# Kernel optimization log

Hardware: AMD Instinct MI355X
Metric: run time of the kernel (lower is better)

Reference implementation:

```python
import jax, jax.numpy as jnp
import numpy as np


def setup_inputs() -> dict:
    key = jax.random.key(0)
    k1, k2 = jax.random.split(key)
    input = jax.random.normal(k1, (4, 2048, 2048), dtype=jnp.float32)
    target = jax.random.normal(k2, (4, 2048, 2048), dtype=jnp.float32) * 2.0 + 0.5
    return {"input": input, "target": target}


def _hist_match(source, template):
    """JAX histogram matching, equivalent to the numpy unique/cumsum/interp
    version for inputs with distinct values (true for continuous random data).

    For each source element x, its empirical quantile is
        q(x) = count(source <= x) / N  == s_quantiles[bin_idx] in the numpy code,
    computed via sort + searchsorted(side='right').
    The template CDF is the sorted template paired with quantiles (j+1)/M,
    matching cumsum(t_counts)/M at each (unique) value.
    """
    src = source.ravel()
    tmpl_sorted = jnp.sort(template.ravel())
    N = src.shape[0]
    M = tmpl_sorted.shape[0]
    s_sorted = jnp.sort(src)
    # rank of each element among all source elements (count <= x)
    ranks = jnp.searchsorted(s_sorted, src, side='right')
    s_q = ranks.astype(jnp.float32) / jnp.float32(N)
    t_q = jnp.arange(1, M + 1, dtype=jnp.float32) / jnp.float32(M)
    matched = jnp.interp(s_q, t_q, tmpl_sorted)
    return matched.reshape(source.shape)


def reference(input, target):
    # hist_match_torch.forward: matched histogram (non-differentiable in original)
    matched = jax.lax.stop_gradient(_hist_match(input, target))
    # HistogramLoss: (matched - input)^2 summed / numel
    loss = jnp.mean((matched - input) ** 2)
    # original forward returns `input`; the meaningful computed quantities are
    # the matched tensor and the loss, so we return both.
    return matched, loss
```

## Files before the change

### kernel.cpp

```cpp
#include <hip/hip_runtime.h>
#include <cstdint>


#define NBINS    8192u
#define HGX      640u
#define MGX      2048u
#define KIN      2048u
#define KTG      4096u

__device__ __forceinline__ void bin_and_frac(float x, unsigned& b, float& frac) {
    float d = __builtin_fmaf(x, 256.0f, 4096.0f);
    d = fminf(fmaxf(d, 0.0f), 8191.999f);
    unsigned bb = (unsigned)d;
    b = bb;
    frac = d - (float)bb;
}

__global__ void hist_kernel(const float* __restrict__ in, const float* __restrict__ tg,
                            unsigned* __restrict__ H, unsigned n8) {
    __shared__ unsigned h[NBINS];
    for (unsigned i = threadIdx.x; i < NBINS; i += 256) h[i] = 0;
    __syncthreads();
    const float* x = blockIdx.y ? tg : in;
    unsigned* Hh = H + blockIdx.y * NBINS;
    unsigned stride = gridDim.x * 256;
    for (unsigned i = blockIdx.x * 256 + threadIdx.x; i < n8; i += stride) {
        float4 a0 = ((const float4*)x)[2 * i];
        float4 a1 = ((const float4*)x)[2 * i + 1];
        float xs[8] = {a0.x, a0.y, a0.z, a0.w, a1.x, a1.y, a1.z, a1.w};
        #pragma unroll
        for (int k = 0; k < 8; k++) {
            unsigned b; float f;
            bin_and_frac(xs[k], b, f);
            atomicAdd(&h[b], 1u);
        }
    }
    __syncthreads();
    for (unsigned i = threadIdx.x; i < NBINS; i += 256) {
        unsigned v = h[i];
        if (v) atomicAdd(&Hh[i], v);
    }
}

__global__ void scan_kernel(const unsigned* __restrict__ H, unsigned* __restrict__ C) {
    __shared__ unsigned s[1024];
    const unsigned* h = H + blockIdx.x * NBINS;
    unsigned* c = C + blockIdx.x * (NBINS + 1);
    unsigned base = threadIdx.x * 8;
    unsigned v[8]; unsigned own = 0;
    #pragma unroll
    for (int k = 0; k < 8; k++) { v[k] = h[base + k]; own += v[k]; }
    s[threadIdx.x] = own; __syncthreads();
    for (unsigned off = 1; off < 1024; off <<= 1) {
        unsigned t = (threadIdx.x >= off) ? s[threadIdx.x - off] : 0u;
        __syncthreads();
        s[threadIdx.x] += t;
        __syncthreads();
    }
    unsigned ex = s[threadIdx.x] - own;
    #pragma unroll
    for (int k = 0; k < 8; k++) { unsigned t = v[k]; c[base + k] = ex; ex += t; }
    if (threadIdx.x == 1023) c[NBINS] = s[1023];
}

__global__ void buildAB_kernel(const unsigned* __restrict__ Cin, const unsigned* __restrict__ Ctg,
                               float2* __restrict__ AB, int* __restrict__ hdr, unsigned n) {
    unsigned b = blockIdx.x * blockDim.x + threadIdx.x;
    if (b >= NBINS) return;
    unsigned r0 = Cin[b], r1 = Cin[b + 1];
    if (r1 <= KIN) atomicMax(&hdr[0], (int)b);
    if (r0 >= n - KIN) atomicMin(&hdr[1], (int)b);
    unsigned t0 = Ctg[b], t1 = Ctg[b + 1];
    if (t1 <= KTG) atomicMax(&hdr[2], (int)b);
    if (t0 >= n - KTG) atomicMin(&hdr[3], (int)b);
    if (r1 == r0) { AB[b] = make_float2(0.f, 0.f); return; }
    const float w = 32.0f / (float)NBINS;
    float v[2];
    unsigned rr[2] = {r0, r1};
    #pragma unroll
    for (int k = 0; k < 2; k++) {
        unsigned r = rr[k]; if (r > n - 1) r = n - 1;
        unsigned lo = 0, hi = NBINS;
        while (hi - lo > 1) { unsigned mid = (lo + hi) >> 1; if (Ctg[mid] <= r) lo = mid; else hi = mid; }
        unsigned c0 = Ctg[lo], c1 = Ctg[lo + 1];
        v[k] = -16.0f + (float)lo * w + w * ((float)(r - c0 + 1) / (float)(c1 - c0));
    }
    AB[b] = make_float2(v[0], v[1] - v[0]);
}

__global__ void exact_target_kernel(const float* __restrict__ tg_lo, const float* __restrict__ tg_hi,
                                    const unsigned* __restrict__ ctrs,
                                    float* __restrict__ Tlo, float* __restrict__ Thi) {
    __shared__ __align__(16) float v[KTG];
    int side = blockIdx.y;
    const float* src = side ? tg_hi : tg_lo;
    unsigned m = ctrs[side ? 3 : 2];
    if (m > KTG) m = KTG;
    float sgn = side ? -1.f : 1.f;
    for (unsigned k = threadIdx.x; k < m; k += 1024) v[k] = sgn * src[k];
    __syncthreads();
    unsigned j = blockIdx.x * 1024 + threadIdx.x;
    if (j >= m) return;
    float y = v[j];
    unsigned lt = 0, le = 0;
    unsigned m4 = m & ~3u;
    for (unsigned k = 0; k < m4; k += 4) {
        float4 z = *(const float4*)&v[k];
        lt += (z.x < y) + (z.y < y) + (z.z < y) + (z.w < y);
        le += (z.x <= y) + (z.y <= y) + (z.z <= y) + (z.w <= y);
    }
    for (unsigned k = m4; k < m; k++) { lt += (v[k] < y); le += (v[k] <= y); }
    float yo = sgn * y;
    if (side) {
        for (unsigned idx = KTG - le; idx < KTG - lt; idx++) Thi[idx] = yo;
    } else {
        for (unsigned r = lt; r < le; r++) Tlo[r] = yo;
    }
}

__global__ void matchcollect_kernel(const float* __restrict__ input, const float* __restrict__ target,
                                    const float2* __restrict__ AB, const int* __restrict__ hdr,
                                    float* __restrict__ vlo, unsigned* __restrict__ ilo,
                                    float* __restrict__ vhi, unsigned* __restrict__ ihi,
                                    float* __restrict__ tg_lo, float* __restrict__ tg_hi,
                                    unsigned* __restrict__ ctrs,
                                    float* __restrict__ out, float* __restrict__ bpart,
                                    unsigned n) {
    unsigned n8 = n >> 3;
    unsigned stride = gridDim.x * 256;
    unsigned i0 = blockIdx.x * 256 + threadIdx.x;

    if (blockIdx.y == 1) {
        int blo = hdr[2], bhi = hdr[3];
        for (unsigned i = i0; i < n8; i += stride) {
            float4 a0 = ((const float4*)target)[2 * i];
            float4 a1 = ((const float4*)target)[2 * i + 1];
            float xs[8] = {a0.x, a0.y, a0.z, a0.w, a1.x, a1.y, a1.z, a1.w};
            unsigned b[8];
            bool lo8[8], hi8[8];
            bool any = false;
            #pragma unroll
            for (int k = 0; k < 8; k++) {
                float f;
                bin_and_frac(xs[k], b[k], f);
                lo8[k] = ((int)b[k] <= blo);
                hi8[k] = ((int)b[k] >= bhi);
                any = any || lo8[k] || hi8[k];
            }
            if (any) {
                #pragma unroll
                for (int k = 0; k < 8; k++) {
                    if (lo8[k]) { unsigned p = atomicAdd(&ctrs[2], 1u); tg_lo[p] = xs[k]; }
                    else if (hi8[k]) { unsigned p = atomicAdd(&ctrs[3], 1u); tg_hi[p] = xs[k]; }
                }
            }
        }
        return;
    }

    int blo = hdr[0], bhi = hdr[1];
    float acc = 0.f;
    for (unsigned i = i0; i < n8; i += stride) {
        float4 a0 = ((const float4*)input)[2 * i];
        float4 a1 = ((const float4*)input)[2 * i + 1];
        float xs[8] = {a0.x, a0.y, a0.z, a0.w, a1.x, a1.y, a1.z, a1.w};
        unsigned b[8]; float fr[8];
        #pragma unroll
        for (int k = 0; k < 8; k++) bin_and_frac(xs[k], b[k], fr[k]);
        float2 ab[8];
        #pragma unroll
        for (int k = 0; k < 8; k++) ab[k] = AB[b[k]];
        bool tl[8]; bool any = false;
        #pragma unroll
        for (int k = 0; k < 8; k++) {
            tl[k] = ((int)b[k] <= blo) || ((int)b[k] >= bhi);
            any = any || tl[k];
        }
        float m[8];
        #pragma unroll
        for (int k = 0; k < 8; k++) {
            m[k] = __builtin_fmaf(ab[k].y, fr[k], ab[k].x);
            float d = tl[k] ? 0.f : (m[k] - xs[k]);
            acc = __builtin_fmaf(d, d, acc);
        }
        ((float4*)out)[2 * i]     = make_float4(m[0], m[1], m[2], m[3]);
        ((float4*)out)[2 * i + 1] = make_float4(m[4], m[5], m[6], m[7]);
        if (any) {
            #pragma unroll
            for (int k = 0; k < 8; k++) {
                if (!tl[k]) continue;
                if ((int)b[k] <= blo) { unsigned p = atomicAdd(&ctrs[0], 1u); vlo[p] = xs[k]; ilo[p] = 8 * i + k; }
                else                  { unsigned p = atomicAdd(&ctrs[1], 1u); vhi[p] = xs[k]; ihi[p] = 8 * i + k; }
            }
        }
    }
    #pragma unroll
    for (int off = 32; off > 0; off >>= 1) acc += __shfl_down(acc, off, 64);
    __shared__ float wsum[4];
    int wv = threadIdx.x >> 6;
    if ((threadIdx.x & 63) == 0) wsum[wv] = acc;
    __syncthreads();
    if (threadIdx.x == 0)
        bpart[blockIdx.x] = wsum[0] + wsum[1] + wsum[2] + wsum[3];
}

__global__ void loss_reduce_kernel(const float* __restrict__ bpart, float* __restrict__ loss,
                                   unsigned nb, unsigned n) {
    float s = 0.f;
    for (unsigned i = threadIdx.x; i < nb; i += 1024) s += bpart[i];
    #pragma unroll
    for (int off = 32; off > 0; off >>= 1) s += __shfl_down(s, off, 64);
    __shared__ float ws[16];
    int w = threadIdx.x >> 6;
    if ((threadIdx.x & 63) == 0) ws[w] = s;
    __syncthreads();
    if (threadIdx.x == 0) {
        float t = 0.f;
        #pragma unroll
        for (int k = 0; k < 16; k++) t += ws[k];
        *loss = t * (1.0f / (float)n);
    }
}

__global__ void exact_input_kernel(const float* __restrict__ in_lo_v, const unsigned* __restrict__ in_lo_i,
                                   const float* __restrict__ in_hi_v, const unsigned* __restrict__ in_hi_i,
                                   const unsigned* __restrict__ ctrs,
                                   const float* __restrict__ Tlo, const float* __restrict__ Thi,
                                   float* __restrict__ out, float* __restrict__ loss, unsigned n) {
    __shared__ __align__(16) float v[KIN];
    int side = blockIdx.y;
    const float* sv = side ? in_hi_v : in_lo_v;
    const unsigned* si = side ? in_hi_i : in_lo_i;
    unsigned m = ctrs[side ? 1 : 0];
    if (m > KIN) m = KIN;
    float sgn = side ? -1.f : 1.f;
    for (unsigned k = threadIdx.x; k < m; k += 1024) v[k] = sgn * sv[k];
    __syncthreads();
    unsigned j = blockIdx.x * 1024 + threadIdx.x;
    float d2 = 0.f;
    if (j < m) {
        float y = v[j];
        unsigned lt = 0, le = 0;
        unsigned m4 = m & ~3u;
        for (unsigned k = 0; k < m4; k += 4) {
            float4 z = *(const float4*)&v[k];
            lt += (z.x < y) + (z.y < y) + (z.z < y) + (z.w < y);
            le += (z.x <= y) + (z.y <= y) + (z.z <= y) + (z.w <= y);
        }
        for (unsigned k = m4; k < m; k++) { lt += (v[k] < y); le += (v[k] <= y); }
        float mv = side ? Thi[KTG - 1 - lt] : Tlo[le - 1];
        float x = sgn * y;
        out[si[j]] = mv;
        float d = mv - x;
        d2 = d * d;
    }
    #pragma unroll
    for (int off = 32; off > 0; off >>= 1) d2 += __shfl_down(d2, off, 64);
    if ((threadIdx.x & 63) == 0 && d2 != 0.f)
        atomicAdd(loss, d2 * (1.0f / (float)n));
}

extern "C" void kernel_launch(void* const* d_in, const int* in_sizes, int n_in,
                              void* d_out, int out_size, void* d_ws, size_t ws_size,
                              hipStream_t stream) {
    const float* input  = (const float*)d_in[0];
    const float* target = (const float*)d_in[1];
    unsigned n = (unsigned)in_sizes[0];
    float* out  = (float*)d_out;
    float* loss = out + n;

    char* wsb = (char*)d_ws;
    unsigned* H    = (unsigned*)(wsb);
    unsigned* Cin  = (unsigned*)(wsb + 64 * 1024);
    unsigned* Ctg  = Cin + (NBINS + 1);
    float2*   AB   = (float2*)  (wsb + 160 * 1024);
    int*      hdr  = (int*)     (wsb + 224 * 1024);
    unsigned* ctrs = (unsigned*)(wsb + 224 * 1024 + 64);
    float*    bpart= (float*)   (wsb + 224 * 1024 + 128);
    char*     tails= wsb + 240 * 1024;
    float*    in_lo_v = (float*)   (tails);
    unsigned* in_lo_i = (unsigned*)(tails + KIN * 4);
    float*    in_hi_v = (float*)   (tails + KIN * 8);
    unsigned* in_hi_i = (unsigned*)(tails + KIN * 12);
    float*    tg_lo   = (float*)   (tails + KIN * 16);
    float*    tg_hi   = (float*)   (tails + KIN * 16 + KTG * 4);
    float*    Tlo     = (float*)   (tails + KIN * 16 + KTG * 8);
    float*    Thi     = (float*)   (tails + KIN * 16 + KTG * 12);

    (void)hipMemsetAsync(H, 0, 2 * NBINS * 4, stream);
    (void)hipMemsetAsync(ctrs, 0, 16, stream);
    (void)hipMemsetAsync(&hdr[0], 0, 4, stream);
    (void)hipMemsetAsync(&hdr[1], 0x7F, 4, stream);
    (void)hipMemsetAsync(&hdr[2], 0, 4, stream);
    (void)hipMemsetAsync(&hdr[3], 0x7F, 4, stream);
    (void)hipMemsetAsync(loss, 0, 4, stream);

    unsigned n8 = n >> 3;

    hist_kernel<<<dim3(HGX, 2), 256, 0, stream>>>(input, target, H, n8);
    scan_kernel<<<2, 1024, 0, stream>>>(H, Cin);
    buildAB_kernel<<<NBINS / 256, 256, 0, stream>>>(Cin, Ctg, AB, hdr, n);

    matchcollect_kernel<<<dim3(MGX, 2), 256, 0, stream>>>(input, target, AB, hdr,
                                                          in_lo_v, in_lo_i, in_hi_v, in_hi_i,
                                                          tg_lo, tg_hi, ctrs, out, bpart, n);
    loss_reduce_kernel<<<1, 1024, 0, stream>>>(bpart, loss, MGX, n);
    exact_target_kernel<<<dim3((KTG + 1023) / 1024, 2), 1024, 0, stream>>>(tg_lo, tg_hi, ctrs, Tlo, Thi);
    exact_input_kernel<<<dim3((KIN + 1023) / 1024, 2), 1024, 0, stream>>>(in_lo_v, in_lo_i, in_hi_v, in_hi_i,
                                                                          ctrs, Tlo, Thi, out, loss, n);
}
```

Measured before the change: 538.2 us.

## Stage AB table in LDS, widen per-thread work, merge header memsets

The match kernel now copies the 8192-entry AB lookup table into shared memory once per block, so the per-element gathers hit LDS instead of global memory. Both the histogram and match kernels move to 512-thread blocks, each thread handling 16 elements, with smaller grids and launch bounds. The min-reductions in buildAB become max on 8192-b, which lets all header and counter fields be cleared with a single zero memset, and each wave writes its own loss partial without a block-level shared-memory reduction. The cost is a 64KB shared-memory fill per block and lower occupancy from the larger LDS footprint.

```diff
diff --git a/kernel.cpp b/kernel.cpp
--- a/kernel.cpp
+++ b/kernel.cpp
@@ -3,8 +3,8 @@
 
 
 #define NBINS    8192u
-#define HGX      640u
-#define MGX      2048u
+#define HGX      512u
+#define MGX      512u
 #define KIN      2048u
 #define KTG      4096u
 
@@ -16,27 +16,29 @@
     frac = d - (float)bb;
 }
 
-__global__ void hist_kernel(const float* __restrict__ in, const float* __restrict__ tg,
-                            unsigned* __restrict__ H, unsigned n8) {
+__global__ __launch_bounds__(512, 8) void hist_kernel(const float* __restrict__ in,
+                                                      const float* __restrict__ tg,
+                                                      unsigned* __restrict__ H, unsigned n16) {
     __shared__ unsigned h[NBINS];
-    for (unsigned i = threadIdx.x; i < NBINS; i += 256) h[i] = 0;
+    for (unsigned i = threadIdx.x; i < NBINS; i += 512) h[i] = 0;
     __syncthreads();
     const float* x = blockIdx.y ? tg : in;
     unsigned* Hh = H + blockIdx.y * NBINS;
-    unsigned stride = gridDim.x * 256;
-    for (unsigned i = blockIdx.x * 256 + threadIdx.x; i < n8; i += stride) {
-        float4 a0 = ((const float4*)x)[2 * i];
-        float4 a1 = ((const float4*)x)[2 * i + 1];
-        float xs[8] = {a0.x, a0.y, a0.z, a0.w, a1.x, a1.y, a1.z, a1.w};
-        #pragma unroll
-        for (int k = 0; k < 8; k++) {
+    unsigned stride = gridDim.x * 512;
+    for (unsigned i = blockIdx.x * 512 + threadIdx.x; i < n16; i += stride) {
+        const float4* p = (const float4*)x + 4u * i;
+        float4 a0 = p[0], a1 = p[1], a2 = p[2], a3 = p[3];
+        float xs[16] = {a0.x, a0.y, a0.z, a0.w, a1.x, a1.y, a1.z, a1.w,
+                        a2.x, a2.y, a2.z, a2.w, a3.x, a3.y, a3.z, a3.w};
+        #pragma unroll
+        for (int k = 0; k < 16; k++) {
             unsigned b; float f;
             bin_and_frac(xs[k], b, f);
             atomicAdd(&h[b], 1u);
         }
     }
     __syncthreads();
-    for (unsigned i = threadIdx.x; i < NBINS; i += 256) {
+    for (unsigned i = threadIdx.x; i < NBINS; i += 512) {
         unsigned v = h[i];
         if (v) atomicAdd(&Hh[i], v);
     }
@@ -69,10 +71,10 @@
     if (b >= NBINS) return;
     unsigned r0 = Cin[b], r1 = Cin[b + 1];
     if (r1 <= KIN) atomicMax(&hdr[0], (int)b);
-    if (r0 >= n - KIN) atomicMin(&hdr[1], (int)b);
+    if (r0 >= n - KIN) atomicMax(&hdr[1], (int)(8192u - b));
     unsigned t0 = Ctg[b], t1 = Ctg[b + 1];
     if (t1 <= KTG) atomicMax(&hdr[2], (int)b);
-    if (t0 >= n - KTG) atomicMin(&hdr[3], (int)b);
+    if (t0 >= n - KTG) atomicMax(&hdr[3], (int)(8192u - b));
     if (r1 == r0) { AB[b] = make_float2(0.f, 0.f); return; }
     const float w = 32.0f / (float)NBINS;
     float v[2];
@@ -118,90 +120,94 @@
     }
 }
 
-__global__ void matchcollect_kernel(const float* __restrict__ input, const float* __restrict__ target,
-                                    const float2* __restrict__ AB, const int* __restrict__ hdr,
-                                    float* __restrict__ vlo, unsigned* __restrict__ ilo,
-                                    float* __restrict__ vhi, unsigned* __restrict__ ihi,
-                                    float* __restrict__ tg_lo, float* __restrict__ tg_hi,
-                                    unsigned* __restrict__ ctrs,
-                                    float* __restrict__ out, float* __restrict__ bpart,
-                                    unsigned n) {
-    unsigned n8 = n >> 3;
-    unsigned stride = gridDim.x * 256;
-    unsigned i0 = blockIdx.x * 256 + threadIdx.x;
+__global__ __launch_bounds__(512, 4) void matchcollect_kernel(
+        const float* __restrict__ input, const float* __restrict__ target,
+        const float2* __restrict__ AB, const int* __restrict__ hdr,
+        float* __restrict__ vlo, unsigned* __restrict__ ilo,
+        float* __restrict__ vhi, unsigned* __restrict__ ihi,
+        float* __restrict__ tg_lo, float* __restrict__ tg_hi,
+        unsigned* __restrict__ ctrs,
+        float* __restrict__ out, float* __restrict__ bpart,
+        unsigned n) {
+    __shared__ float2 sAB[NBINS];
+    unsigned n16 = n >> 4;
+    unsigned stride = gridDim.x * 512;
+    unsigned i0 = blockIdx.x * 512 + threadIdx.x;
 
     if (blockIdx.y == 1) {
-        int blo = hdr[2], bhi = hdr[3];
-        for (unsigned i = i0; i < n8; i += stride) {
-            float4 a0 = ((const float4*)target)[2 * i];
-            float4 a1 = ((const float4*)target)[2 * i + 1];
-            float xs[8] = {a0.x, a0.y, a0.z, a0.w, a1.x, a1.y, a1.z, a1.w};
-            unsigned b[8];
-            bool lo8[8], hi8[8];
-            bool any = false;
+        int blo = hdr[2], bhi = 8192 - hdr[3];
+        for (unsigned i = i0; i < n16; i += stride) {
+            const float4* p = (const float4*)target + 4u * i;
+            float4 a0 = p[0], a1 = p[1], a2 = p[2], a3 = p[3];
+            float xs[16] = {a0.x, a0.y, a0.z, a0.w, a1.x, a1.y, a1.z, a1.w,
+                            a2.x, a2.y, a2.z, a2.w, a3.x, a3.y, a3.z, a3.w};
+            unsigned b[16]; bool lo16[16], hi16[16]; bool any = false;
             #pragma unroll
-            for (int k = 0; k < 8; k++) {
+            for (int k = 0; k < 16; k++) {
                 float f;
                 bin_and_frac(xs[k], b[k], f);
-                lo8[k] = ((int)b[k] <= blo);
-                hi8[k] = ((int)b[k] >= bhi);
-                any = any || lo8[k] || hi8[k];
+                lo16[k] = ((int)b[k] <= blo);
+                hi16[k] = ((int)b[k] >= bhi);
+                any = any || lo16[k] || hi16[k];
             }
             if (any) {
                 #pragma unroll
-                for (int k = 0; k < 8; k++) {
-                    if (lo8[k]) { unsigned p = atomicAdd(&ctrs[2], 1u); tg_lo[p] = xs[k]; }
-                    else if (hi8[k]) { unsigned p = atomicAdd(&ctrs[3], 1u); tg_hi[p] = xs[k]; }
+                for (int k = 0; k < 16; k++) {
+                    if (lo16[k]) { unsigned p2 = atomicAdd(&ctrs[2], 1u); tg_lo[p2] = xs[k]; }
+                    else if (hi16[k]) { unsigned p2 = atomicAdd(&ctrs[3], 1u); tg_hi[p2] = xs[k]; }
                 }
             }
         }
         return;
     }
 
-    int blo = hdr[0], bhi = hdr[1];
+    for (unsigned j = threadIdx.x; j < NBINS; j += 512) sAB[j] = AB[j];
+    __syncthreads();
+
+    int blo = hdr[0], bhi = 8192 - hdr[1];
     float acc = 0.f;
-    for (unsigned i = i0; i < n8; i += stride) {
-        float4 a0 = ((const float4*)input)[2 * i];
-        float4 a1 = ((const float4*)input)[2 * i + 1];
-        float xs[8] = {a0.x, a0.y, a0.z, a0.w, a1.x, a1.y, a1.z, a1.w};
-        unsigned b[8]; float fr[8];
-        #pragma unroll
-        for (int k = 0; k < 8; k++) bin_and_frac(xs[k], b[k], fr[k]);
-        float2 ab[8];
-        #pragma unroll
-        for (int k = 0; k < 8; k++) ab[k] = AB[b[k]];
-        bool tl[8]; bool any = false;
-        #pragma unroll
-        for (int k = 0; k < 8; k++) {
+    for (unsigned i = i0; i < n16; i += stride) {
+        const float4* p = (const float4*)input + 4u * i;
+        float4 a0 = p[0], a1 = p[1], a2 = p[2], a3 = p[3];
+        float xs[16] = {a0.x, a0.y, a0.z, a0.w, a1.x, a1.y, a1.z, a1.w,
+                        a2.x, a2.y, a2.z, a2.w, a3.x, a3.y, a3.z, a3.w};
+        unsigned b[16]; float fr[16];
+        #pragma unroll
+        for (int k = 0; k < 16; k++) bin_and_frac(xs[k], b[k], fr[k]);
+        float2 ab[16];
+        #pragma unroll
+        for (int k = 0; k < 16; k++) ab[k] = sAB[b[k]];
+        bool tl[16]; bool any = false;
+        #pragma unroll
+        for (int k = 0; k < 16; k++) {
             tl[k] = ((int)b[k] <= blo) || ((int)b[k] >= bhi);
             any = any || tl[k];
         }
-        float m[8];
-        #pragma unroll
-        for (int k = 0; k < 8; k++) {
+        float m[16];
+        #pragma unroll
+        for (int k = 0; k < 16; k++) {
             m[k] = __builtin_fmaf(ab[k].y, fr[k], ab[k].x);
             float d = tl[k] ? 0.f : (m[k] - xs[k]);
             acc = __builtin_fmaf(d, d, acc);
         }
-        ((float4*)out)[2 * i]     = make_float4(m[0], m[1], m[2], m[3]);
-        ((float4*)out)[2 * i + 1] = make_float4(m[4], m[5], m[6], m[7]);
+        float4* q = (float4*)out + 4u * i;
+        q[0] = make_float4(m[0],  m[1],  m[2],  m[3]);
+        q[1] = make_float4(m[4],  m[5],  m[6],  m[7]);
+        q[2] = make_float4(m[8],  m[9],  m[10], m[11]);
+        q[3] = make_float4(m[12], m[13], m[14], m[15]);
         if (any) {
             #pragma unroll
-            for (int k = 0; k < 8; k++) {
+            for (int k = 0; k < 16; k++) {
                 if (!tl[k]) continue;
-                if ((int)b[k] <= blo) { unsigned p = atomicAdd(&ctrs[0], 1u); vlo[p] = xs[k]; ilo[p] = 8 * i + k; }
-                else                  { unsigned p = atomicAdd(&ctrs[1], 1u); vhi[p] = xs[k]; ihi[p] = 8 * i + k; }
+                if ((int)b[k] <= blo) { unsigned p2 = atomicAdd(&ctrs[0], 1u); vlo[p2] = xs[k]; ilo[p2] = 16 * i + k; }
+                else                  { unsigned p2 = atomicAdd(&ctrs[1], 1u); vhi[p2] = xs[k]; ihi[p2] = 16 * i + k; }
             }
         }
     }
     #pragma unroll
     for (int off = 32; off > 0; off >>= 1) acc += __shfl_down(acc, off, 64);
-    __shared__ float wsum[4];
-    int wv = threadIdx.x >> 6;
-    if ((threadIdx.x & 63) == 0) wsum[wv] = acc;
-    __syncthreads();
-    if (threadIdx.x == 0)
-        bpart[blockIdx.x] = wsum[0] + wsum[1] + wsum[2] + wsum[3];
+    if ((threadIdx.x & 63) == 0)
+        bpart[blockIdx.x * 8 + (threadIdx.x >> 6)] = acc;
 }
 
 __global__ void loss_reduce_kernel(const float* __restrict__ bpart, float* __restrict__ loss,
@@ -274,10 +280,11 @@
     unsigned* Cin  = (unsigned*)(wsb + 64 * 1024);
     unsigned* Ctg  = Cin + (NBINS + 1);
     float2*   AB   = (float2*)  (wsb + 160 * 1024);
-    int*      hdr  = (int*)     (wsb + 224 * 1024);
-    unsigned* ctrs = (unsigned*)(wsb + 224 * 1024 + 64);
-    float*    bpart= (float*)   (wsb + 224 * 1024 + 128);
-    char*     tails= wsb + 240 * 1024;
+    char*     aux  = wsb + 224 * 1024;
+    int*      hdr  = (int*)     (aux);
+    unsigned* ctrs = (unsigned*)(aux + 16);
+    float*    bpart= (float*)   (aux + 64);
+    char*     tails= aux + 64 + 16384 + 64;
     float*    in_lo_v = (float*)   (tails);
     unsigned* in_lo_i = (unsigned*)(tails + KIN * 4);
     float*    in_hi_v = (float*)   (tails + KIN * 8);
@@ -288,23 +295,19 @@
     float*    Thi     = (float*)   (tails + KIN * 16 + KTG * 12);
 
     (void)hipMemsetAsync(H, 0, 2 * NBINS * 4, stream);
-    (void)hipMemsetAsync(ctrs, 0, 16, stream);
-    (void)hipMemsetAsync(&hdr[0], 0, 4, stream);
-    (void)hipMemsetAsync(&hdr[1], 0x7F, 4, stream);
-    (void)hipMemsetAsync(&hdr[2], 0, 4, stream);
-    (void)hipMemsetAsync(&hdr[3], 0x7F, 4, stream);
+    (void)hipMemsetAsync(hdr, 0, 32, stream);
     (void)hipMemsetAsync(loss, 0, 4, stream);
 
-    unsigned n8 = n >> 3;
-
-    hist_kernel<<<dim3(HGX, 2), 256, 0, stream>>>(input, target, H, n8);
+    unsigned n16 = n >> 4;
+
+    hist_kernel<<<dim3(HGX, 2), 512, 0, stream>>>(input, target, H, n16);
     scan_kernel<<<2, 1024, 0, stream>>>(H, Cin);
     buildAB_kernel<<<NBINS / 256, 256, 0, stream>>>(Cin, Ctg, AB, hdr, n);
 
-    matchcollect_kernel<<<dim3(MGX, 2), 256, 0, stream>>>(input, target, AB, hdr,
+    matchcollect_kernel<<<dim3(MGX, 2), 512, 0, stream>>>(input, target, AB, hdr,
                                                           in_lo_v, in_lo_i, in_hi_v, in_hi_i,
                                                           tg_lo, tg_hi, ctrs, out, bpart, n);
-    loss_reduce_kernel<<<1, 1024, 0, stream>>>(bpart, loss, MGX, n);
+    loss_reduce_kernel<<<1, 1024, 0, stream>>>(bpart, loss, MGX * 8, n);
     exact_target_kernel<<<dim3((KTG + 1023) / 1024, 2), 1024, 0, stream>>>(tg_lo, tg_hi, ctrs, Tlo, Thi);
     exact_input_kernel<<<dim3((KIN + 1023) / 1024, 2), 1024, 0, stream>>>(in_lo_v, in_lo_i, in_hi_v, in_hi_i,
                                                                           ctrs, Tlo, Thi, out, loss, n);
```

Result: faster. 525.4 us (-2.4%).

## Unroll grid-stride loops by two, merge memsets, per-wave partial sums

Applied to the files above, without the earlier changes.

The histogram and match/collect loops now process two strided chunks per iteration, issuing both loads before compute so more memory requests are in flight. The histogram kernel uses 512-thread blocks with a smaller grid, and launch bounds are added. The min-bin header encoding is changed to atomicMax on (8192-b), which lets one zero memset replace several small ones. The block-level shared-memory reduction in match is replaced by writing per-wave partials, so the loss reduction reads four times as many values.

```diff
diff --git a/kernel.cpp b/kernel.cpp
--- a/kernel.cpp
+++ b/kernel.cpp
@@ -3,7 +3,7 @@
 
 
 #define NBINS    8192u
-#define HGX      640u
+#define HGX      512u
 #define MGX      2048u
 #define KIN      2048u
 #define KTG      4096u
@@ -16,27 +16,37 @@
     frac = d - (float)bb;
 }
 
-__global__ void hist_kernel(const float* __restrict__ in, const float* __restrict__ tg,
-                            unsigned* __restrict__ H, unsigned n8) {
+__device__ __forceinline__ void hist8(float4 A0, float4 A1, unsigned* h) {
+    float xs[8] = {A0.x, A0.y, A0.z, A0.w, A1.x, A1.y, A1.z, A1.w};
+    #pragma unroll
+    for (int k = 0; k < 8; k++) {
+        unsigned b; float f;
+        bin_and_frac(xs[k], b, f);
+        atomicAdd(&h[b], 1u);
+    }
+}
+
+__global__ __launch_bounds__(512, 8) void hist_kernel(const float* __restrict__ in,
+                                                      const float* __restrict__ tg,
+                                                      unsigned* __restrict__ H, unsigned n8) {
     __shared__ unsigned h[NBINS];
-    for (unsigned i = threadIdx.x; i < NBINS; i += 256) h[i] = 0;
+    for (unsigned i = threadIdx.x; i < NBINS; i += 512) h[i] = 0;
     __syncthreads();
     const float* x = blockIdx.y ? tg : in;
     unsigned* Hh = H + blockIdx.y * NBINS;
-    unsigned stride = gridDim.x * 256;
-    for (unsigned i = blockIdx.x * 256 + threadIdx.x; i < n8; i += stride) {
+    unsigned stride = gridDim.x * 512, stride2 = stride * 2;
+    for (unsigned i = blockIdx.x * 512 + threadIdx.x; i < n8; i += stride2) {
+        unsigned j = i + stride;
+        unsigned jj = (j < n8) ? j : i;
         float4 a0 = ((const float4*)x)[2 * i];
         float4 a1 = ((const float4*)x)[2 * i + 1];
-        float xs[8] = {a0.x, a0.y, a0.z, a0.w, a1.x, a1.y, a1.z, a1.w};
-        #pragma unroll
-        for (int k = 0; k < 8; k++) {
-            unsigned b; float f;
-            bin_and_frac(xs[k], b, f);
-            atomicAdd(&h[b], 1u);
-        }
-    }
-    __syncthreads();
-    for (unsigned i = threadIdx.x; i < NBINS; i += 256) {
+        float4 c0 = ((const float4*)x)[2 * jj];
+        float4 c1 = ((const float4*)x)[2 * jj + 1];
+        hist8(a0, a1, h);
+        if (j < n8) hist8(c0, c1, h);
+    }
+    __syncthreads();
+    for (unsigned i = threadIdx.x; i < NBINS; i += 512) {
         unsigned v = h[i];
         if (v) atomicAdd(&Hh[i], v);
     }
@@ -69,10 +79,10 @@
     if (b >= NBINS) return;
     unsigned r0 = Cin[b], r1 = Cin[b + 1];
     if (r1 <= KIN) atomicMax(&hdr[0], (int)b);
-    if (r0 >= n - KIN) atomicMin(&hdr[1], (int)b);
+    if (r0 >= n - KIN) atomicMax(&hdr[1], (int)(8192u - b));
     unsigned t0 = Ctg[b], t1 = Ctg[b + 1];
     if (t1 <= KTG) atomicMax(&hdr[2], (int)b);
-    if (t0 >= n - KTG) atomicMin(&hdr[3], (int)b);
+    if (t0 >= n - KTG) atomicMax(&hdr[3], (int)(8192u - b));
     if (r1 == r0) { AB[b] = make_float2(0.f, 0.f); return; }
     const float w = 32.0f / (float)NBINS;
     float v[2];
@@ -118,90 +128,108 @@
     }
 }
 
-__global__ void matchcollect_kernel(const float* __restrict__ input, const float* __restrict__ target,
-                                    const float2* __restrict__ AB, const int* __restrict__ hdr,
-                                    float* __restrict__ vlo, unsigned* __restrict__ ilo,
-                                    float* __restrict__ vhi, unsigned* __restrict__ ihi,
-                                    float* __restrict__ tg_lo, float* __restrict__ tg_hi,
-                                    unsigned* __restrict__ ctrs,
-                                    float* __restrict__ out, float* __restrict__ bpart,
-                                    unsigned n) {
+__device__ __forceinline__ void collect8(float4 A0, float4 A1, int blo, int bhi,
+                                         float* __restrict__ tg_lo, float* __restrict__ tg_hi,
+                                         unsigned* __restrict__ ctrs) {
+    float xs[8] = {A0.x, A0.y, A0.z, A0.w, A1.x, A1.y, A1.z, A1.w};
+    bool lo8[8], hi8[8]; bool any = false;
+    #pragma unroll
+    for (int k = 0; k < 8; k++) {
+        unsigned b; float f;
+        bin_and_frac(xs[k], b, f);
+        lo8[k] = ((int)b <= blo);
+        hi8[k] = ((int)b >= bhi);
+        any = any || lo8[k] || hi8[k];
+    }
+    if (any) {
+        #pragma unroll
+        for (int k = 0; k < 8; k++) {
+            if (lo8[k]) { unsigned p = atomicAdd(&ctrs[2], 1u); tg_lo[p] = xs[k]; }
+            else if (hi8[k]) { unsigned p = atomicAdd(&ctrs[3], 1u); tg_hi[p] = xs[k]; }
+        }
+    }
+}
+
+__device__ __forceinline__ float match8(float4 A0, float4 A1, unsigned i,
+                                        const float2* __restrict__ AB, int blo, int bhi,
+                                        float* __restrict__ out,
+                                        float* __restrict__ vlo, unsigned* __restrict__ ilo,
+                                        float* __restrict__ vhi, unsigned* __restrict__ ihi,
+                                        unsigned* __restrict__ ctrs) {
+    float xs[8] = {A0.x, A0.y, A0.z, A0.w, A1.x, A1.y, A1.z, A1.w};
+    unsigned b[8]; float fr[8];
+    #pragma unroll
+    for (int k = 0; k < 8; k++) bin_and_frac(xs[k], b[k], fr[k]);
+    float2 ab[8];
+    #pragma unroll
+    for (int k = 0; k < 8; k++) ab[k] = AB[b[k]];
+    float m[8]; bool tl[8]; bool any = false; float acc = 0.f;
+    #pragma unroll
+    for (int k = 0; k < 8; k++) {
+        m[k] = __builtin_fmaf(ab[k].y, fr[k], ab[k].x);
+        tl[k] = ((int)b[k] <= blo) || ((int)b[k] >= bhi);
+        any = any || tl[k];
+        float d = tl[k] ? 0.f : (m[k] - xs[k]);
+        acc = __builtin_fmaf(d, d, acc);
+    }
+    ((float4*)out)[2 * i]     = make_float4(m[0], m[1], m[2], m[3]);
+    ((float4*)out)[2 * i + 1] = make_float4(m[4], m[5], m[6], m[7]);
+    if (any) {
+        #pragma unroll
+        for (int k = 0; k < 8; k++) {
+            if (!tl[k]) continue;
+            if ((int)b[k] <= blo) { unsigned p = atomicAdd(&ctrs[0], 1u); vlo[p] = xs[k]; ilo[p] = 8 * i + k; }
+            else                  { unsigned p = atomicAdd(&ctrs[1], 1u); vhi[p] = xs[k]; ihi[p] = 8 * i + k; }
+        }
+    }
+    return acc;
+}
+
+__global__ __launch_bounds__(256, 8) void matchcollect_kernel(
+        const float* __restrict__ input, const float* __restrict__ target,
+        const float2* __restrict__ AB, const int* __restrict__ hdr,
+        float* __restrict__ vlo, unsigned* __restrict__ ilo,
+        float* __restrict__ vhi, unsigned* __restrict__ ihi,
+        float* __restrict__ tg_lo, float* __restrict__ tg_hi,
+        unsigned* __restrict__ ctrs,
+        float* __restrict__ out, float* __restrict__ bpart,
+        unsigned n) {
     unsigned n8 = n >> 3;
-    unsigned stride = gridDim.x * 256;
+    unsigned stride = gridDim.x * 256, stride2 = stride * 2;
     unsigned i0 = blockIdx.x * 256 + threadIdx.x;
 
     if (blockIdx.y == 1) {
-        int blo = hdr[2], bhi = hdr[3];
-        for (unsigned i = i0; i < n8; i += stride) {
+        int blo = hdr[2], bhi = 8192 - hdr[3];
+        for (unsigned i = i0; i < n8; i += stride2) {
+            unsigned j = i + stride;
+            unsigned jj = (j < n8) ? j : i;
             float4 a0 = ((const float4*)target)[2 * i];
             float4 a1 = ((const float4*)target)[2 * i + 1];
-            float xs[8] = {a0.x, a0.y, a0.z, a0.w, a1.x, a1.y, a1.z, a1.w};
-            unsigned b[8];
-            bool lo8[8], hi8[8];
-            bool any = false;
-            #pragma unroll
-            for (int k = 0; k < 8; k++) {
-                float f;
-                bin_and_frac(xs[k], b[k], f);
-                lo8[k] = ((int)b[k] <= blo);
-                hi8[k] = ((int)b[k] >= bhi);
-                any = any || lo8[k] || hi8[k];
-            }
-            if (any) {
-                #pragma unroll
-                for (int k = 0; k < 8; k++) {
-                    if (lo8[k]) { unsigned p = atomicAdd(&ctrs[2], 1u); tg_lo[p] = xs[k]; }
-                    else if (hi8[k]) { unsigned p = atomicAdd(&ctrs[3], 1u); tg_hi[p] = xs[k]; }
-                }
-            }
+            float4 c0 = ((const float4*)target)[2 * jj];
+            float4 c1 = ((const float4*)target)[2 * jj + 1];
+            collect8(a0, a1, blo, bhi, tg_lo, tg_hi, ctrs);
+            if (j < n8) collect8(c0, c1, blo, bhi, tg_lo, tg_hi, ctrs);
         }
         return;
     }
 
-    int blo = hdr[0], bhi = hdr[1];
+    int blo = hdr[0], bhi = 8192 - hdr[1];
     float acc = 0.f;
-    for (unsigned i = i0; i < n8; i += stride) {
+    for (unsigned i = i0; i < n8; i += stride2) {
+        unsigned j = i + stride;
+        unsigned jj = (j < n8) ? j : i;
         float4 a0 = ((const float4*)input)[2 * i];
         float4 a1 = ((const float4*)input)[2 * i + 1];
-        float xs[8] = {a0.x, a0.y, a0.z, a0.w, a1.x, a1.y, a1.z, a1.w};
-        unsigned b[8]; float fr[8];
-        #pragma unroll
-        for (int k = 0; k < 8; k++) bin_and_frac(xs[k], b[k], fr[k]);
-        float2 ab[8];
-        #pragma unroll
-        for (int k = 0; k < 8; k++) ab[k] = AB[b[k]];
-        bool tl[8]; bool any = false;
-        #pragma unroll
-        for (int k = 0; k < 8; k++) {
-            tl[k] = ((int)b[k] <= blo) || ((int)b[k] >= bhi);
-            any = any || tl[k];
-        }
-        float m[8];
-        #pragma unroll
-        for (int k = 0; k < 8; k++) {
-            m[k] = __builtin_fmaf(ab[k].y, fr[k], ab[k].x);
-            float d = tl[k] ? 0.f : (m[k] - xs[k]);
-            acc = __builtin_fmaf(d, d, acc);
-        }
-        ((float4*)out)[2 * i]     = make_float4(m[0], m[1], m[2], m[3]);
-        ((float4*)out)[2 * i + 1] = make_float4(m[4], m[5], m[6], m[7]);
-        if (any) {
-            #pragma unroll
-            for (int k = 0; k < 8; k++) {
-                if (!tl[k]) continue;
-                if ((int)b[k] <= blo) { unsigned p = atomicAdd(&ctrs[0], 1u); vlo[p] = xs[k]; ilo[p] = 8 * i + k; }
-                else                  { unsigned p = atomicAdd(&ctrs[1], 1u); vhi[p] = xs[k]; ihi[p] = 8 * i + k; }
-            }
-        }
+        float4 c0 = ((const float4*)input)[2 * jj];
+        float4 c1 = ((const float4*)input)[2 * jj + 1];
+        acc += match8(a0, a1, i, AB, blo, bhi, out, vlo, ilo, vhi, ihi, ctrs);
+        if (j < n8)
+            acc += match8(c0, c1, j, AB, blo, bhi, out, vlo, ilo, vhi, ihi, ctrs);
     }
     #pragma unroll
     for (int off = 32; off > 0; off >>= 1) acc += __shfl_down(acc, off, 64);
-    __shared__ float wsum[4];
-    int wv = threadIdx.x >> 6;
-    if ((threadIdx.x & 63) == 0) wsum[wv] = acc;
-    __syncthreads();
-    if (threadIdx.x == 0)
-        bpart[blockIdx.x] = wsum[0] + wsum[1] + wsum[2] + wsum[3];
+    if ((threadIdx.x & 63) == 0)
+        bpart[blockIdx.x * 4 + (threadIdx.x >> 6)] = acc;
 }
 
 __global__ void loss_reduce_kernel(const float* __restrict__ bpart, float* __restrict__ loss,
@@ -274,10 +302,11 @@
     unsigned* Cin  = (unsigned*)(wsb + 64 * 1024);
     unsigned* Ctg  = Cin + (NBINS + 1);
     float2*   AB   = (float2*)  (wsb + 160 * 1024);
-    int*      hdr  = (int*)     (wsb + 224 * 1024);
-    unsigned* ctrs = (unsigned*)(wsb + 224 * 1024 + 64);
-    float*    bpart= (float*)   (wsb + 224 * 1024 + 128);
-    char*     tails= wsb + 240 * 1024;
+    char*     aux  = wsb + 224 * 1024;
+    int*      hdr  = (int*)     (aux);
+    unsigned* ctrs = (unsigned*)(aux + 16);
+    float*    bpart= (float*)   (aux + 64);
+    char*     tails= aux + 64 + 65536 + 64;
     float*    in_lo_v = (float*)   (tails);
     unsigned* in_lo_i = (unsigned*)(tails + KIN * 4);
     float*    in_hi_v = (float*)   (tails + KIN * 8);
@@ -288,23 +317,19 @@
     float*    Thi     = (float*)   (tails + KIN * 16 + KTG * 12);
 
     (void)hipMemsetAsync(H, 0, 2 * NBINS * 4, stream);
-    (void)hipMemsetAsync(ctrs, 0, 16, stream);
-    (void)hipMemsetAsync(&hdr[0], 0, 4, stream);
-    (void)hipMemsetAsync(&hdr[1], 0x7F, 4, stream);
-    (void)hipMemsetAsync(&hdr[2], 0, 4, stream);
-    (void)hipMemsetAsync(&hdr[3], 0x7F, 4, stream);
+    (void)hipMemsetAsync(hdr, 0, 32, stream);
     (void)hipMemsetAsync(loss, 0, 4, stream);
 
     unsigned n8 = n >> 3;
 
-    hist_kernel<<<dim3(HGX, 2), 256, 0, stream>>>(input, target, H, n8);
+    hist_kernel<<<dim3(HGX, 2), 512, 0, stream>>>(input, target, H, n8);
     scan_kernel<<<2, 1024, 0, stream>>>(H, Cin);
     buildAB_kernel<<<NBINS / 256, 256, 0, stream>>>(Cin, Ctg, AB, hdr, n);
 
     matchcollect_kernel<<<dim3(MGX, 2), 256, 0, stream>>>(input, target, AB, hdr,
                                                           in_lo_v, in_lo_i, in_hi_v, in_hi_i,
                                                           tg_lo, tg_hi, ctrs, out, bpart, n);
-    loss_reduce_kernel<<<1, 1024, 0, stream>>>(bpart, loss, MGX, n);
+    loss_reduce_kernel<<<1, 1024, 0, stream>>>(bpart, loss, MGX * 4, n);
     exact_target_kernel<<<dim3((KTG + 1023) / 1024, 2), 1024, 0, stream>>>(tg_lo, tg_hi, ctrs, Tlo, Thi);
     exact_input_kernel<<<dim3((KIN + 1023) / 1024, 2), 1024, 0, stream>>>(in_lo_v, in_lo_i, in_hi_v, in_hi_i,
                                                                           ctrs, Tlo, Thi, out, loss, n);
```

New measurement: 524.0 us. -2.6%, faster.
